# Optimization experiments

Measured on AMD Instinct MI355X. Metric: run time of the kernel, lower is better.

Reference implementation:

```python
import jax, jax.numpy as jnp
import numpy as np

B, T, D = 2048, 60, 6
H, F, O = 64, 10, 1


def setup_inputs() -> dict:
    key = jax.random.key(0)
    ks = jax.random.split(key, 16)
    w = lambda k, shape, s=0.1: jax.random.normal(k, shape, jnp.float32) * s
    return {
        "x": jax.random.normal(ks[0], (B, T, D), jnp.float32),
        "W_i": w(ks[1], (D, H)), "U_i": w(ks[2], (H, H)), "b_i": jnp.zeros((H,), jnp.float32),
        "W_ste": w(ks[3], (D, H)), "U_ste": w(ks[4], (H, H)), "b_ste": jnp.ones((H,), jnp.float32),
        "W_fre": w(ks[5], (D, F)), "U_fre": w(ks[6], (H, F)), "b_fre": jnp.ones((F,), jnp.float32),
        "W_c": w(ks[7], (D, H)), "U_c": w(ks[8], (H, H)), "b_c": jnp.zeros((H,), jnp.float32),
        "W_o": w(ks[9], (D, H)), "U_o": w(ks[10], (H, H)), "b_o": jnp.zeros((H,), jnp.float32),
        "U_a": w(ks[11], (F, 1)), "b_a": jnp.zeros((H,), jnp.float32),
        "W_p": w(ks[12], (H, O)), "b_p": jnp.zeros((O,), jnp.float32),
    }


def _hsig(v):
    # torch.nn.Hardsigmoid: relu6(x + 3) / 6
    return jnp.clip(v / 6.0 + 0.5, 0.0, 1.0)


def reference(x, W_i, U_i, b_i, W_ste, U_ste, b_ste, W_fre, U_fre, b_fre,
              W_c, U_c, b_c, W_o, U_o, b_o, U_a, b_a, W_p, b_p):
    b, t_len, _ = x.shape
    h_dim = W_i.shape[1]
    f_dim = W_fre.shape[1]
    freq = jnp.arange(f_dim, dtype=x.dtype) / f_dim  # (F,)
    ua = U_a[:, 0]  # (F,)

    def step(carry, x_t):
        h, S_re, S_im, t = carry
        i = _hsig(x_t @ W_i + b_i + h @ U_i)              # (B,H)
        ste = _hsig(x_t @ W_ste + b_ste + h @ U_ste)      # (B,H)
        fre = _hsig(x_t @ W_fre + b_fre + h @ U_fre)      # (B,F)
        f = ste[:, :, None] * fre[:, None, :]             # (B,H,F)
        c = i * jnp.tanh(x_t @ W_c + b_c + h @ U_c)       # (B,H)
        t = t + 1.0
        omega = (2.0 * jnp.pi) * t * freq                  # (F,)
        S_re = f * S_re + c[:, :, None] * jnp.cos(omega)   # (B,H,F)
        S_im = f * S_im + c[:, :, None] * jnp.sin(omega)   # (B,H,F)
        A = S_re * S_re + S_im * S_im                      # (B,H,F)
        a = jnp.tanh(jnp.einsum('bhf,f->bh', A, ua) + b_a)
        o = _hsig(x_t @ W_o + b_o + h @ U_o)
        h = o * a
        return (h, S_re, S_im, t), None

    init = (jnp.zeros((b, h_dim), x.dtype),
            jnp.zeros((b, h_dim, f_dim), x.dtype),
            jnp.zeros((b, h_dim, f_dim), x.dtype),
            jnp.asarray(0.0, x.dtype))
    (h, _, _, _), _ = jax.lax.scan(step, init, jnp.swapaxes(x, 0, 1))
    # original returns p from the last timestep only
    return h @ W_p + b_p
```

## Files before the change

kernel.cpp:

```cpp
#include <hip/hip_runtime.h>


#define BB 2048
#define TT 60
#define DD 6
#define HH 64
#define FF 10
#define NB 8

#define XS 968
#define HSK 72
#define ZC 68

typedef short bf16x8 __attribute__((ext_vector_type(8)));
typedef float f32x4  __attribute__((ext_vector_type(4)));

__device__ __forceinline__ unsigned short f2bf(float f) {
    union { float f; unsigned u; } v; v.f = f;
    unsigned r = v.u + 0x7fffu + ((v.u >> 16) & 1u);
    return (unsigned short)(r >> 16);
}
__device__ __forceinline__ float bf2f(unsigned short b) {
    union { unsigned u; float f; } v; v.u = ((unsigned)b) << 16; return v.f;
}
__device__ __forceinline__ float hsig_f(float v) {
    return __builtin_amdgcn_fmed3f(fmaf(v, 0.16666666666666666f, 0.5f), 0.0f, 1.0f);
}
__device__ __forceinline__ float tanh_f(float x) {
    float xc = fminf(fmaxf(x, -12.0f), 12.0f);
    float e  = __builtin_amdgcn_exp2f(xc * 2.8853900817779268f);
    return (e - 1.0f) * __builtin_amdgcn_rcpf(e + 1.0f);
}
__device__ __forceinline__ float uni(float v) {
    return __int_as_float(__builtin_amdgcn_readfirstlane(__float_as_int(v)));
}
__device__ __forceinline__ void pinv(bf16x8& v) { asm volatile("" : "+v"(v)); }

__global__ __launch_bounds__(512, 1)
void sfm_kernel(
    const float* __restrict__ x,
    const float* __restrict__ W_i,  const float* __restrict__ U_i,  const float* __restrict__ b_i,
    const float* __restrict__ W_ste,const float* __restrict__ U_ste,const float* __restrict__ b_ste,
    const float* __restrict__ W_fre,const float* __restrict__ U_fre,const float* __restrict__ b_fre,
    const float* __restrict__ W_c,  const float* __restrict__ U_c,  const float* __restrict__ b_c,
    const float* __restrict__ W_o,  const float* __restrict__ U_o,  const float* __restrict__ b_o,
    const float* __restrict__ U_a,  const float* __restrict__ b_a,
    const float* __restrict__ W_p,  const float* __restrict__ b_p,
    float* __restrict__ out)
{
    const int tid  = threadIdx.x;
    const int lane = tid & 63;
    const int wave = tid >> 6;
    const int q    = lane >> 4;
    const int n16  = lane & 15;
    const int b0   = blockIdx.x * NB;

    __shared__ __align__(16) unsigned short xsp[NB * XS];
    __shared__ __align__(16) unsigned short hsp2[16 * HSK];
    __shared__ __align__(16) float zt[4 * 16 * ZC];
    __shared__ __align__(16) float fb[NB * 12];
    __shared__ __align__(16) float ctab[10 * 10 * 2];
    __shared__ float cstabB[10 * 2];
    __shared__ float red[8][8];

    if (tid < NB * TT) {
        const float* xg = x + (size_t)b0 * (TT * DD) + tid * DD;
        const int b = tid / TT, s = tid - b * TT;
        unsigned short* dst = &xsp[b * XS + s * 16];
        #pragma unroll
        for (int d = 0; d < DD; ++d) {
            const float v = xg[d];
            const unsigned short hb = f2bf(v);
            dst[d]     = hb;
            dst[8 + d] = f2bf(v - bf2f(hb));
        }
        dst[6] = 0x3F80; dst[7] = 0;
        dst[14] = 0; dst[15] = 0;
    }
    if (tid < 10) {
        const float CTc[10] = { 1.0f,  0.8090169943749475f,  0.30901699437494745f,
                               -0.30901699437494745f, -0.8090169943749475f, -1.0f,
                               -0.8090169943749475f, -0.30901699437494745f,
                                0.30901699437494745f,  0.8090169943749475f };
        const float STc[10] = { 0.0f,  0.5877852522924731f,  0.9510565162951535f,
                                0.9510565162951535f,  0.5877852522924731f,  0.0f,
                               -0.5877852522924731f, -0.9510565162951535f,
                               -0.9510565162951535f, -0.5877852522924731f };
        float cc = 0.0f, ss = 0.0f;
        #pragma unroll
        for (int j = 0; j < 10; ++j) if (tid == j) { cc = CTc[j]; ss = STc[j]; }
        cstabB[tid * 2] = cc; cstabB[tid * 2 + 1] = ss;
    }
    for (int i = tid; i < 16 * HSK; i += 512) hsp2[i] = 0;
    __syncthreads();
    if (tid < 100) {
        const int mm = tid / 10, ff = tid - mm * 10;
        const int idx = (ff * mm) % 10;
        ctab[tid * 2]     = cstabB[idx * 2];
        ctab[tid * 2 + 1] = cstabB[idx * 2 + 1];
    }

    const int NTILE = (wave == 7) ? 3 : 2;
    bf16x8 Ah[3][3], Al[3][3];
    #pragma unroll
    for (int t = 0; t < 3; ++t) {
        if (t >= NTILE) continue;
        const bool isfre = (wave == 7 && t == 2);
        const int gt = 2 * wave + t;
        const int g  = gt >> 2, mt = gt & 3;
        const int col = mt * 16 + n16;
        const float* Ug = (g == 0) ? U_i : (g == 1) ? U_ste : (g == 2) ? U_c : U_o;
        const float* Wg = (g == 0) ? W_i : (g == 1) ? W_ste : (g == 2) ? W_c : W_o;
        const float* bg = (g == 0) ? b_i : (g == 1) ? b_ste : (g == 2) ? b_c : b_o;
        #pragma unroll
        for (int c = 0; c < 3; ++c) {
            #pragma unroll
            for (int j = 0; j < 8; ++j) {
                const int kv = c * 32 + q * 8 + j;
                float v = 0.0f;
                if (!isfre) {
                    if      (kv < 64)  v = Ug[kv * HH + col];
                    else if (kv < 70)  v = Wg[(kv - 64) * HH + col];
                    else if (kv == 70) v = bg[col];
                } else if (n16 < FF) {
                    if      (kv < 64)  v = U_fre[kv * FF + n16];
                    else if (kv < 70)  v = W_fre[(kv - 64) * FF + n16];
                    else if (kv == 70) v = b_fre[n16];
                }
                const unsigned short hb = f2bf(v);
                Ah[t][c][j] = (short)hb;
                Al[t][c][j] = (short)f2bf(v - bf2f(hb));
            }
            pinv(Ah[t][c]); pinv(Al[t][c]);
        }
    }

    const int pb = tid & 7;
    const int pc = tid >> 3;
    const float bav = b_a[pc];
    const float wpv = W_p[pc];
    const float bpv = uni(b_p[0]);
    float uav[FF];
    #pragma unroll
    for (int f = 0; f < FF; ++f) uav[f] = uni(U_a[f]);

    float Sre[FF], Sim[FF];
    #pragma unroll
    for (int f = 0; f < FF; ++f) { Sre[f] = 0.0f; Sim[f] = 0.0f; }
    float hv = 0.0f;

    const unsigned short* hrp = &hsp2[n16 * HSK];
    const unsigned short* xrp = &xsp[(n16 & 7) * XS + (n16 >> 3) * 8];

    __syncthreads();

    int m = 1;
    for (int s = 0; s < TT; ++s) {
        const bf16x8 B0 = *(const bf16x8*)&hrp[q * 8];
        const bf16x8 B1 = *(const bf16x8*)&hrp[32 + q * 8];
        const bf16x8 xv = *(const bf16x8*)&xrp[s * 16];
        const bf16x8 zf = {0, 0, 0, 0, 0, 0, 0, 0};
        const bf16x8 B2 = (q == 0) ? xv : zf;

        f32x4 acc[3];
        #pragma unroll
        for (int t = 0; t < 3; ++t) {
            if (t >= NTILE) continue;
            f32x4 a = {0.0f, 0.0f, 0.0f, 0.0f};
            a = __builtin_amdgcn_mfma_f32_16x16x32_bf16(Ah[t][0], B0, a, 0, 0, 0);
            a = __builtin_amdgcn_mfma_f32_16x16x32_bf16(Al[t][0], B0, a, 0, 0, 0);
            a = __builtin_amdgcn_mfma_f32_16x16x32_bf16(Ah[t][1], B1, a, 0, 0, 0);
            a = __builtin_amdgcn_mfma_f32_16x16x32_bf16(Al[t][1], B1, a, 0, 0, 0);
            a = __builtin_amdgcn_mfma_f32_16x16x32_bf16(Ah[t][2], B2, a, 0, 0, 0);
            a = __builtin_amdgcn_mfma_f32_16x16x32_bf16(Al[t][2], B2, a, 0, 0, 0);
            acc[t] = a;
        }

        #pragma unroll
        for (int t = 0; t < 2; ++t) {
            const int gt = 2 * wave + t;
            const int g  = gt >> 2, mt = gt & 3;
            *(f32x4*)&zt[(g * 16 + n16) * ZC + mt * 16 + q * 4] = acc[t];
        }
        if (wave == 7) {
            f32x4 af;
            #pragma unroll
            for (int r = 0; r < 4; ++r)
                af[r] = acc[2][r] + __shfl_xor(acc[2][r], 8, 64);
            if (n16 < 8) {
                #pragma unroll
                for (int r = 0; r < 4; ++r) {
                    const int f = q * 4 + r;
                    if (f < FF) fb[n16 * 12 + f] = af[r];
                }
            }
        }
        __syncthreads();

        const float zi = zt[(0 * 16 + pb) * ZC + pc] + zt[(0 * 16 + pb + 8) * ZC + pc];
        const float zs = zt[(1 * 16 + pb) * ZC + pc] + zt[(1 * 16 + pb + 8) * ZC + pc];
        const float zc = zt[(2 * 16 + pb) * ZC + pc] + zt[(2 * 16 + pb + 8) * ZC + pc];
        const float zo = zt[(3 * 16 + pb) * ZC + pc] + zt[(3 * 16 + pb + 8) * ZC + pc];

        float fr[FF];
        #pragma unroll
        for (int f = 0; f < FF; ++f) fr[f] = hsig_f(fb[pb * 12 + f]);

        const float iv  = hsig_f(zi);
        const float stv = hsig_f(zs);
        const float ov  = hsig_f(zo);
        const float cv  = iv * tanh_f(zc);

        const float* tp = &ctab[m * 20];
        float aacc0 = bav, aacc1 = 0.0f;
        #pragma unroll
        for (int f = 0; f < FF; ++f) {
            const float2 tv = *(const float2*)&tp[f * 2];
            const float fc = stv * fr[f];
            Sre[f] = fmaf(fc, Sre[f], cv * tv.x);
            Sim[f] = fmaf(fc, Sim[f], cv * tv.y);
            const float A = fmaf(Sim[f], Sim[f], Sre[f] * Sre[f]);
            if (f & 1) aacc1 = fmaf(A, uav[f], aacc1);
            else       aacc0 = fmaf(A, uav[f], aacc0);
        }
        hv = ov * tanh_f(aacc0 + aacc1);

        {
            const unsigned short hb = f2bf(hv);
            hsp2[pb * HSK + pc]       = hb;
            hsp2[(8 + pb) * HSK + pc] = f2bf(hv - bf2f(hb));
        }
        if (++m == 10) m = 0;
        __syncthreads();
    }

    float val = hv * wpv;
    val += __shfl_xor(val, 8, 64);
    val += __shfl_xor(val, 16, 64);
    val += __shfl_xor(val, 32, 64);
    if (lane < 8) red[wave][lane] = val;
    __syncthreads();
    if (tid < NB) {
        float acc = bpv;
        #pragma unroll
        for (int w = 0; w < 8; ++w) acc += red[w][tid];
        out[b0 + tid] = acc;
    }
}

extern "C" void kernel_launch(void* const* d_in, const int* in_sizes, int n_in,
                              void* d_out, int out_size, void* d_ws, size_t ws_size,
                              hipStream_t stream) {
    (void)in_sizes; (void)n_in; (void)d_ws; (void)ws_size; (void)out_size;
    const float* x     = (const float*)d_in[0];
    const float* W_i   = (const float*)d_in[1];
    const float* U_i   = (const float*)d_in[2];
    const float* b_i   = (const float*)d_in[3];
    const float* W_ste = (const float*)d_in[4];
    const float* U_ste = (const float*)d_in[5];
    const float* b_ste = (const float*)d_in[6];
    const float* W_fre = (const float*)d_in[7];
    const float* U_fre = (const float*)d_in[8];
    const float* b_fre = (const float*)d_in[9];
    const float* W_c   = (const float*)d_in[10];
    const float* U_c   = (const float*)d_in[11];
    const float* b_c   = (const float*)d_in[12];
    const float* W_o   = (const float*)d_in[13];
    const float* U_o   = (const float*)d_in[14];
    const float* b_o   = (const float*)d_in[15];
    const float* U_a   = (const float*)d_in[16];
    const float* b_a   = (const float*)d_in[17];
    const float* W_p   = (const float*)d_in[18];
    const float* b_p   = (const float*)d_in[19];

    sfm_kernel<<<BB / NB, 512, 0, stream>>>(
        x, W_i, U_i, b_i, W_ste, U_ste, b_ste, W_fre, U_fre, b_fre,
        W_c, U_c, b_c, W_o, U_o, b_o, U_a, b_a, W_p, b_p, (float*)d_out);
}
```

Measured before the change: 157.1 us.

## Shrink block to four waves, each owning one hidden column tile across all gates

```diff
diff --git a/kernel.cpp b/kernel.cpp
--- a/kernel.cpp
+++ b/kernel.cpp
@@ -10,7 +10,6 @@
 
 #define XS 968
 #define HSK 72
-#define ZC 68
 
 typedef short bf16x8 __attribute__((ext_vector_type(8)));
 typedef float f32x4  __attribute__((ext_vector_type(4)));
@@ -36,7 +35,8 @@
 }
 __device__ __forceinline__ void pinv(bf16x8& v) { asm volatile("" : "+v"(v)); }
 
-__global__ __launch_bounds__(512, 1)
+__global__ __launch_bounds__(256)
+__attribute__((amdgpu_waves_per_eu(1, 1)))
 void sfm_kernel(
     const float* __restrict__ x,
     const float* __restrict__ W_i,  const float* __restrict__ U_i,  const float* __restrict__ b_i,
@@ -57,15 +57,14 @@
 
     __shared__ __align__(16) unsigned short xsp[NB * XS];
     __shared__ __align__(16) unsigned short hsp2[16 * HSK];
-    __shared__ __align__(16) float zt[4 * 16 * ZC];
-    __shared__ __align__(16) float fb[NB * 12];
+    __shared__ __align__(16) float fbw[4][8][16];
     __shared__ __align__(16) float ctab[10 * 10 * 2];
     __shared__ float cstabB[10 * 2];
-    __shared__ float red[8][8];
-
-    if (tid < NB * TT) {
-        const float* xg = x + (size_t)b0 * (TT * DD) + tid * DD;
-        const int b = tid / TT, s = tid - b * TT;
+    __shared__ float red[4][NB];
+
+    for (int item = tid; item < NB * TT; item += 256) {
+        const float* xg = x + (size_t)b0 * (TT * DD) + item * DD;
+        const int b = item / TT, s = item - b * TT;
         unsigned short* dst = &xsp[b * XS + s * 16];
         #pragma unroll
         for (int d = 0; d < DD; ++d) {
@@ -91,7 +90,7 @@
         for (int j = 0; j < 10; ++j) if (tid == j) { cc = CTc[j]; ss = STc[j]; }
         cstabB[tid * 2] = cc; cstabB[tid * 2 + 1] = ss;
     }
-    for (int i = tid; i < 16 * HSK; i += 512) hsp2[i] = 0;
+    for (int i = tid; i < 16 * HSK; i += 256) hsp2[i] = 0;
     __syncthreads();
     if (tid < 100) {
         const int mm = tid / 10, ff = tid - mm * 10;
@@ -100,32 +99,25 @@
         ctab[tid * 2 + 1] = cstabB[idx * 2 + 1];
     }
 
-    const int NTILE = (wave == 7) ? 3 : 2;
-    bf16x8 Ah[3][3], Al[3][3];
+    bf16x8 Ah[5][3], Al[5][3];
     #pragma unroll
-    for (int t = 0; t < 3; ++t) {
-        if (t >= NTILE) continue;
-        const bool isfre = (wave == 7 && t == 2);
-        const int gt = 2 * wave + t;
-        const int g  = gt >> 2, mt = gt & 3;
-        const int col = mt * 16 + n16;
-        const float* Ug = (g == 0) ? U_i : (g == 1) ? U_ste : (g == 2) ? U_c : U_o;
-        const float* Wg = (g == 0) ? W_i : (g == 1) ? W_ste : (g == 2) ? W_c : W_o;
-        const float* bg = (g == 0) ? b_i : (g == 1) ? b_ste : (g == 2) ? b_c : b_o;
+    for (int t = 0; t < 5; ++t) {
+        const float* Up = (t==0)?U_i:(t==1)?U_ste:(t==2)?U_c:(t==3)?U_o:U_fre;
+        const float* Wp = (t==0)?W_i:(t==1)?W_ste:(t==2)?W_c:(t==3)?W_o:W_fre;
+        const float* bp = (t==0)?b_i:(t==1)?b_ste:(t==2)?b_c:(t==3)?b_o:b_fre;
+        const int nd  = (t < 4) ? HH : FF;
+        const int col = (t < 4) ? (wave * 16 + n16) : n16;
+        const bool ok = (t < 4) || (n16 < FF);
         #pragma unroll
         for (int c = 0; c < 3; ++c) {
             #pragma unroll
             for (int j = 0; j < 8; ++j) {
                 const int kv = c * 32 + q * 8 + j;
                 float v = 0.0f;
-                if (!isfre) {
-                    if      (kv < 64)  v = Ug[kv * HH + col];
-                    else if (kv < 70)  v = Wg[(kv - 64) * HH + col];
-                    else if (kv == 70) v = bg[col];
-                } else if (n16 < FF) {
-                    if      (kv < 64)  v = U_fre[kv * FF + n16];
-                    else if (kv < 70)  v = W_fre[(kv - 64) * FF + n16];
-                    else if (kv == 70) v = b_fre[n16];
+                if (ok) {
+                    if      (kv < 64)  v = Up[kv * nd + col];
+                    else if (kv < 70)  v = Wp[(kv - 64) * nd + col];
+                    else if (kv == 70) v = bp[col];
                 }
                 const unsigned short hb = f2bf(v);
                 Ah[t][c][j] = (short)hb;
@@ -135,22 +127,23 @@
         }
     }
 
-    const int pb = tid & 7;
-    const int pc = tid >> 3;
-    const float bav = b_a[pc];
-    const float wpv = W_p[pc];
+    const int b   = n16 & 7;
+    const int hi3 = n16 >> 3;
+    const int hc0 = wave * 16 + q * 4 + hi3 * 2;
+    const float ba0 = b_a[hc0], ba1 = b_a[hc0 + 1];
+    const float wp0 = W_p[hc0], wp1 = W_p[hc0 + 1];
     const float bpv = uni(b_p[0]);
     float uav[FF];
     #pragma unroll
     for (int f = 0; f < FF; ++f) uav[f] = uni(U_a[f]);
 
-    float Sre[FF], Sim[FF];
+    float Sre0[FF], Sim0[FF], Sre1[FF], Sim1[FF];
     #pragma unroll
-    for (int f = 0; f < FF; ++f) { Sre[f] = 0.0f; Sim[f] = 0.0f; }
-    float hv = 0.0f;
+    for (int f = 0; f < FF; ++f) { Sre0[f]=0.f; Sim0[f]=0.f; Sre1[f]=0.f; Sim1[f]=0.f; }
+    float hv0 = 0.0f, hv1 = 0.0f;
 
     const unsigned short* hrp = &hsp2[n16 * HSK];
-    const unsigned short* xrp = &xsp[(n16 & 7) * XS + (n16 >> 3) * 8];
+    const unsigned short* xrp = &xsp[b * XS + hi3 * 8];
 
     __syncthreads();
 
@@ -159,13 +152,12 @@
         const bf16x8 B0 = *(const bf16x8*)&hrp[q * 8];
         const bf16x8 B1 = *(const bf16x8*)&hrp[32 + q * 8];
         const bf16x8 xv = *(const bf16x8*)&xrp[s * 16];
-        const bf16x8 zf = {0, 0, 0, 0, 0, 0, 0, 0};
-        const bf16x8 B2 = (q == 0) ? xv : zf;
-
-        f32x4 acc[3];
-        #pragma unroll
-        for (int t = 0; t < 3; ++t) {
-            if (t >= NTILE) continue;
+        const bf16x8 zf8 = {0, 0, 0, 0, 0, 0, 0, 0};
+        const bf16x8 B2 = (q == 0) ? xv : zf8;
+
+        f32x4 acc[5];
+        #pragma unroll
+        for (int t = 0; t < 5; ++t) {
             f32x4 a = {0.0f, 0.0f, 0.0f, 0.0f};
             a = __builtin_amdgcn_mfma_f32_16x16x32_bf16(Ah[t][0], B0, a, 0, 0, 0);
             a = __builtin_amdgcn_mfma_f32_16x16x32_bf16(Al[t][0], B0, a, 0, 0, 0);
@@ -176,76 +168,75 @@
             acc[t] = a;
         }
 
-        #pragma unroll
-        for (int t = 0; t < 2; ++t) {
-            const int gt = 2 * wave + t;
-            const int g  = gt >> 2, mt = gt & 3;
-            *(f32x4*)&zt[(g * 16 + n16) * ZC + mt * 16 + q * 4] = acc[t];
-        }
-        if (wave == 7) {
-            f32x4 af;
+        f32x4 z[5];
+        #pragma unroll
+        for (int t = 0; t < 5; ++t) {
             #pragma unroll
             for (int r = 0; r < 4; ++r)
-                af[r] = acc[2][r] + __shfl_xor(acc[2][r], 8, 64);
-            if (n16 < 8) {
-                #pragma unroll
-                for (int r = 0; r < 4; ++r) {
-                    const int f = q * 4 + r;
-                    if (f < FF) fb[n16 * 12 + f] = af[r];
-                }
-            }
-        }
-        __syncthreads();
-
-        const float zi = zt[(0 * 16 + pb) * ZC + pc] + zt[(0 * 16 + pb + 8) * ZC + pc];
-        const float zs = zt[(1 * 16 + pb) * ZC + pc] + zt[(1 * 16 + pb + 8) * ZC + pc];
-        const float zc = zt[(2 * 16 + pb) * ZC + pc] + zt[(2 * 16 + pb + 8) * ZC + pc];
-        const float zo = zt[(3 * 16 + pb) * ZC + pc] + zt[(3 * 16 + pb + 8) * ZC + pc];
-
+                z[t][r] = acc[t][r] + __shfl_xor(acc[t][r], 8, 64);
+        }
+
+        if (n16 < 8) *(f32x4*)&fbw[wave][n16][q * 4] = z[4];
+        asm volatile("" ::: "memory");
+        const f32x4  fA = *(const f32x4*)&fbw[wave][b][0];
+        const f32x4  fB = *(const f32x4*)&fbw[wave][b][4];
+        const float2 fC = *(const float2*)&fbw[wave][b][8];
         float fr[FF];
         #pragma unroll
-        for (int f = 0; f < FF; ++f) fr[f] = hsig_f(fb[pb * 12 + f]);
-
-        const float iv  = hsig_f(zi);
-        const float stv = hsig_f(zs);
-        const float ov  = hsig_f(zo);
-        const float cv  = iv * tanh_f(zc);
+        for (int f = 0; f < 4; ++f) fr[f] = hsig_f(fA[f]);
+        #pragma unroll
+        for (int f = 0; f < 4; ++f) fr[4 + f] = hsig_f(fB[f]);
+        fr[8] = hsig_f(fC.x); fr[9] = hsig_f(fC.y);
+
+        const float zi0 = hi3 ? z[0][2] : z[0][0], zi1 = hi3 ? z[0][3] : z[0][1];
+        const float zs0 = hi3 ? z[1][2] : z[1][0], zs1 = hi3 ? z[1][3] : z[1][1];
+        const float zc0 = hi3 ? z[2][2] : z[2][0], zc1 = hi3 ? z[2][3] : z[2][1];
+        const float zo0 = hi3 ? z[3][2] : z[3][0], zo1 = hi3 ? z[3][3] : z[3][1];
+
+        const float iv0 = hsig_f(zi0), st0 = hsig_f(zs0), ov0 = hsig_f(zo0);
+        const float iv1 = hsig_f(zi1), st1 = hsig_f(zs1), ov1 = hsig_f(zo1);
+        const float cv0 = iv0 * tanh_f(zc0);
+        const float cv1 = iv1 * tanh_f(zc1);
 
         const float* tp = &ctab[m * 20];
-        float aacc0 = bav, aacc1 = 0.0f;
+        float a00 = ba0, a01 = 0.0f, a10 = ba1, a11 = 0.0f;
         #pragma unroll
         for (int f = 0; f < FF; ++f) {
             const float2 tv = *(const float2*)&tp[f * 2];
-            const float fc = stv * fr[f];
-            Sre[f] = fmaf(fc, Sre[f], cv * tv.x);
-            Sim[f] = fmaf(fc, Sim[f], cv * tv.y);
-            const float A = fmaf(Sim[f], Sim[f], Sre[f] * Sre[f]);
-            if (f & 1) aacc1 = fmaf(A, uav[f], aacc1);
-            else       aacc0 = fmaf(A, uav[f], aacc0);
-        }
-        hv = ov * tanh_f(aacc0 + aacc1);
+            const float fc0 = st0 * fr[f];
+            const float fc1 = st1 * fr[f];
+            Sre0[f] = fmaf(fc0, Sre0[f], cv0 * tv.x);
+            Sim0[f] = fmaf(fc0, Sim0[f], cv0 * tv.y);
+            Sre1[f] = fmaf(fc1, Sre1[f], cv1 * tv.x);
+            Sim1[f] = fmaf(fc1, Sim1[f], cv1 * tv.y);
+            const float A0 = fmaf(Sim0[f], Sim0[f], Sre0[f] * Sre0[f]);
+            const float A1 = fmaf(Sim1[f], Sim1[f], Sre1[f] * Sre1[f]);
+            if (f & 1) { a01 = fmaf(A0, uav[f], a01); a11 = fmaf(A1, uav[f], a11); }
+            else       { a00 = fmaf(A0, uav[f], a00); a10 = fmaf(A1, uav[f], a10); }
+        }
+        hv0 = ov0 * tanh_f(a00 + a01);
+        hv1 = ov1 * tanh_f(a10 + a11);
 
         {
-            const unsigned short hb = f2bf(hv);
-            hsp2[pb * HSK + pc]       = hb;
-            hsp2[(8 + pb) * HSK + pc] = f2bf(hv - bf2f(hb));
+            const unsigned short hA = f2bf(hv0);
+            const unsigned short hB = f2bf(hv1);
+            hsp2[b * HSK + hc0]           = hA;
+            hsp2[(8 + b) * HSK + hc0]     = f2bf(hv0 - bf2f(hA));
+            hsp2[b * HSK + hc0 + 1]       = hB;
+            hsp2[(8 + b) * HSK + hc0 + 1] = f2bf(hv1 - bf2f(hB));
         }
         if (++m == 10) m = 0;
         __syncthreads();
     }
 
-    float val = hv * wpv;
+    float val = fmaf(hv0, wp0, hv1 * wp1);
     val += __shfl_xor(val, 8, 64);
     val += __shfl_xor(val, 16, 64);
     val += __shfl_xor(val, 32, 64);
     if (lane < 8) red[wave][lane] = val;
     __syncthreads();
-    if (tid < NB) {
-        float acc = bpv;
-        #pragma unroll
-        for (int w = 0; w < 8; ++w) acc += red[w][tid];
-        out[b0 + tid] = acc;
-    }
+    if (tid < NB)
+        out[b0 + tid] = red[0][tid] + red[1][tid] + red[2][tid] + red[3][tid] + bpv;
 }
 
 extern "C" void kernel_launch(void* const* d_in, const int* in_sizes, int n_in,
@@ -273,7 +264,7 @@
     const float* W_p   = (const float*)d_in[18];
     const float* b_p   = (const float*)d_in[19];
 
-    sfm_kernel<<<BB / NB, 512, 0, stream>>>(
+    sfm_kernel<<<BB / NB, 256, 0, stream>>>(
         x, W_i, U_i, b_i, W_ste, U_ste, b_ste, W_fre, U_fre, b_fre,
         W_c, U_c, b_c, W_o, U_o, b_o, U_a, b_a, W_p, b_p, (float*)d_out);
 }
```

Result: slower. 160.6 us (+2.3%).
